# Kernel optimization log

Measured on AMD Instinct MI355X. Metric: run time of the kernel, lower is better.

The kernel has to match this reference:

```python
import jax, jax.numpy as jnp
from jax import lax
import numpy as np

B, FRAMES, H, W = 8, 128, 64, 64
N_MFCC = 60
VID_FEAT = 196
D = VID_FEAT + N_MFCC   # COMBINE_SIZE = 256
ED = 2 * D              # mamba d_inner = 512
NST = 16                # d_state
DTR = 16                # dt_rank = ceil(D/16)
NL = 4                  # layers per direction
NC = 2                  # num_classes


def setup_inputs() -> dict:
    key = jax.random.key(0)
    ks = iter(jax.random.split(key, 64))
    def rn(shape, s=0.02):
        return jax.random.normal(next(ks), shape, jnp.float32) * s
    inp = {
        'video_input': jax.random.normal(next(ks), (B, FRAMES, 3, H, W), jnp.float32),
        'audio_input': jax.random.normal(next(ks), (B, FRAMES * N_MFCC), jnp.float32),
        'cnn_conv1_w': rn((32, 3, 3, 3), 0.1), 'cnn_conv1_b': jnp.zeros((32,), jnp.float32),
        'cnn_conv2_w': rn((64, 32, 3, 3), 0.05), 'cnn_conv2_b': jnp.zeros((64,), jnp.float32),
        'cnn_fc_w': rn((VID_FEAT, 64), 0.1), 'cnn_fc_b': jnp.zeros((VID_FEAT,), jnp.float32),
    }
    for pref in ('fwd', 'bwd'):
        inp[pref + '_norm_w'] = jnp.ones((NL, D), jnp.float32)
        inp[pref + '_in_proj_w'] = rn((NL, 2 * ED, D))
        inp[pref + '_conv_w'] = rn((NL, ED, 4), 0.1)
        inp[pref + '_conv_b'] = jnp.zeros((NL, ED), jnp.float32)
        inp[pref + '_x_proj_w'] = rn((NL, DTR + 2 * NST, ED))
        inp[pref + '_dt_w'] = rn((NL, ED, DTR), 0.1)
        inp[pref + '_dt_b'] = jnp.zeros((NL, ED), jnp.float32)
        inp[pref + '_A_log'] = jnp.tile(jnp.log(jnp.arange(1, NST + 1, dtype=jnp.float32)), (NL, ED, 1))
        inp[pref + '_D'] = jnp.ones((NL, ED), jnp.float32)
        inp[pref + '_out_proj_w'] = rn((NL, D, ED))
    inp['fc_w'] = rn((D, 2 * D)); inp['fc_b'] = jnp.zeros((D,), jnp.float32)
    inp['fc2_w'] = rn((NC, D)); inp['fc2_b'] = jnp.zeros((NC,), jnp.float32)
    return inp


def _rmsnorm(x, w, eps=1e-5):
    return x * lax.rsqrt(jnp.mean(x * x, -1, keepdims=True) + eps) * w


def _conv2d(x, w, b):
    y = lax.conv_general_dilated(x, w, (1, 1), 'SAME', dimension_numbers=('NCHW', 'OIHW', 'NCHW'))
    return y + b[None, :, None, None]


def _maxpool2(x):
    return lax.reduce_window(x, -jnp.inf, lax.max, (1, 1, 2, 2), (1, 1, 2, 2), 'VALID')


def _video_cnn(x, w1, b1, w2, b2, fw, fb):
    x = _maxpool2(jax.nn.relu(_conv2d(x, w1, b1)))
    x = _maxpool2(jax.nn.relu(_conv2d(x, w2, b2)))
    x = jnp.mean(x, (2, 3))            # global avg pool -> [B*F, 64]
    return x @ fw.T + fb               # [B*F, VID_FEAT]


def _mamba_layer(x, norm_w, in_w, conv_w, conv_b, xp_w, dt_w, dt_b, A_log, Dp, out_w):
    Bsz, L, _ = x.shape
    xn = _rmsnorm(x, norm_w)
    xz = jnp.einsum('bld,ed->ble', xn, in_w)        # [B,L,2*ED]
    xc, z = jnp.split(xz, 2, axis=-1)
    # causal depthwise conv1d, kernel 4
    xpad = jnp.pad(xc, ((0, 0), (3, 0), (0, 0)))
    xc = sum(xpad[:, k:k + L, :] * conv_w[:, k] for k in range(4)) + conv_b
    xc = jax.nn.silu(xc)
    dbc = jnp.einsum('ble,re->blr', xc, xp_w)       # [B,L,DTR+2*NST]
    dt, Bm, Cm = dbc[..., :DTR], dbc[..., DTR:DTR + NST], dbc[..., DTR + NST:]
    delta = jax.nn.softplus(jnp.einsum('blr,er->ble', dt, dt_w) + dt_b)  # [B,L,ED]
    A = -jnp.exp(A_log)                             # [ED,NST]
    dA = jnp.exp(delta[..., None] * A)              # [B,L,ED,NST]
    dBx = delta[..., None] * Bm[:, :, None, :] * xc[..., None]
    def step(h, inp):
        dA_t, dBx_t, c_t = inp
        h = dA_t * h + dBx_t
        return h, jnp.einsum('ben,bn->be', h, c_t)
    h0 = jnp.zeros((Bsz, ED, NST), x.dtype)
    _, ys = lax.scan(step, h0, (dA.transpose(1, 0, 2, 3), dBx.transpose(1, 0, 2, 3), Cm.transpose(1, 0, 2)))
    y = ys.transpose(1, 0, 2) + Dp * xc
    y = y * jax.nn.silu(z)
    return x + jnp.einsum('ble,de->bld', y, out_w)


def _mamba(x, norm_w, in_w, conv_w, conv_b, xp_w, dt_w, dt_b, A_log, Dp, out_w):
    for l in range(NL):
        x = _mamba_layer(x, norm_w[l], in_w[l], conv_w[l], conv_b[l], xp_w[l],
                         dt_w[l], dt_b[l], A_log[l], Dp[l], out_w[l])
    return x


def reference(video_input, audio_input, cnn_conv1_w, cnn_conv1_b, cnn_conv2_w, cnn_conv2_b,
              cnn_fc_w, cnn_fc_b,
              fwd_norm_w, fwd_in_proj_w, fwd_conv_w, fwd_conv_b, fwd_x_proj_w, fwd_dt_w,
              fwd_dt_b, fwd_A_log, fwd_D, fwd_out_proj_w,
              bwd_norm_w, bwd_in_proj_w, bwd_conv_w, bwd_conv_b, bwd_x_proj_w, bwd_dt_w,
              bwd_dt_b, bwd_A_log, bwd_D, bwd_out_proj_w,
              fc_w, fc_b, fc2_w, fc2_b):
    bsz, frames = video_input.shape[0], video_input.shape[1]
    xv = video_input.reshape(bsz * frames, 3, H, W)
    xv = _video_cnn(xv, cnn_conv1_w, cnn_conv1_b, cnn_conv2_w, cnn_conv2_b, cnn_fc_w, cnn_fc_b)
    xv = xv.reshape(bsz, frames, VID_FEAT)
    xa = audio_input.reshape(bsz, -1, N_MFCC)       # [B, frames, N_MFCC]
    xc = jnp.concatenate([xv, xa], axis=-1)         # [B, frames, D]
    xf = _mamba(xc, fwd_norm_w, fwd_in_proj_w, fwd_conv_w, fwd_conv_b, fwd_x_proj_w,
                fwd_dt_w, fwd_dt_b, fwd_A_log, fwd_D, fwd_out_proj_w)
    xb = _mamba(xc[:, ::-1], bwd_norm_w, bwd_in_proj_w, bwd_conv_w, bwd_conv_b, bwd_x_proj_w,
                bwd_dt_w, bwd_dt_b, bwd_A_log, bwd_D, bwd_out_proj_w)[:, ::-1]
    x_last = jnp.concatenate([xf, xb], axis=-1)[:, -1, :]   # [B, 2*D]; dropout = identity (eval)
    x = x_last @ fc_w.T + fc_b
    return x @ fc2_w.T + fc2_b
```

## Files before the change

kernel.cpp:

```cpp
#include <hip/hip_runtime.h>
#include <hip/hip_bf16.h>
#include <cstdint>
#include <cstddef>

#define BATCH 8
#define FRAMES 128
#define TOK (BATCH*FRAMES)
#define NM 60
#define VF 196
#define DD 256
#define EDIM 512
#define NSTATE 16
#define DTRANK 16
#define NLAYER 4

typedef __attribute__((ext_vector_type(8))) short short8v;
typedef __attribute__((ext_vector_type(4))) float f32x4;

__device__ __forceinline__ unsigned short f2bf(float f) {
  unsigned x = __float_as_uint(f);
  unsigned r = (x + 0x7FFFu + ((x >> 16) & 1u)) >> 16;
  return (unsigned short)r;
}
__device__ __forceinline__ float bf2f(unsigned short u) {
  return __uint_as_float((unsigned)u << 16);
}

__global__ void pack_all(const float* __restrict__ ipF, const float* __restrict__ ipR,
                         const float* __restrict__ opF, const float* __restrict__ opR,
                         const float* __restrict__ xpF, const float* __restrict__ xpR,
                         const float* __restrict__ w2, const float* __restrict__ w1,
                         unsigned short* __restrict__ Wip, unsigned short* __restrict__ Wop,
                         unsigned short* __restrict__ Wxp, unsigned short* __restrict__ Wb,
                         unsigned short* __restrict__ Wb1) {
  int id = blockIdx.x * 256 + threadIdx.x;
  if (id < 262144) {
    int dl = id >> 15, r = id & 32767;
    int ntile = r >> 9, kt = (r >> 6) & 7, lane = r & 63;
    int dir = dl >> 2, layer = dl & 3;
    const float* src = (dir ? ipR : ipF) + (size_t)layer * 1024 * 256
                       + (size_t)(ntile * 16 + (lane & 15)) * 256 + kt * 32 + (lane >> 4) * 8;
    unsigned u[4];
#pragma unroll
    for (int p = 0; p < 4; ++p)
      u[p] = (unsigned)f2bf(src[2 * p]) | ((unsigned)f2bf(src[2 * p + 1]) << 16);
    uint4 v = {u[0], u[1], u[2], u[3]};
    *(uint4*)(Wip + (size_t)id * 8) = v;
  } else if (id < 262144 + 131072) {
    int id2 = id - 262144;
    int dl = id2 >> 14, rr = id2 & 16383;
    int ntile = rr >> 10, kt = (rr >> 6) & 15, lane = rr & 63;
    int dir = dl >> 2, layer = dl & 3;
    const float* src = (dir ? opR : opF) + (size_t)layer * 256 * 512
                       + (size_t)(ntile * 16 + (lane & 15)) * 512 + kt * 32 + (lane >> 4) * 8;
    unsigned u[4];
#pragma unroll
    for (int p = 0; p < 4; ++p)
      u[p] = (unsigned)f2bf(src[2 * p]) | ((unsigned)f2bf(src[2 * p + 1]) << 16);
    uint4 v = {u[0], u[1], u[2], u[3]};
    *(uint4*)(Wop + (size_t)id2 * 8) = v;
  } else if (id < 262144 + 131072 + 24576) {
    int id3 = id - 262144 - 131072;
    int dl = id3 / 3072, rr = id3 % 3072;
    int ntile = rr >> 10, kt = (rr >> 6) & 15, lane = rr & 63;
    int dir = dl >> 2, layer = dl & 3;
    const float* src = (dir ? xpR : xpF) + (size_t)layer * 48 * 512
                       + (size_t)(ntile * 16 + (lane & 15)) * 512 + kt * 32 + (lane >> 4) * 8;
    unsigned u[4];
#pragma unroll
    for (int p = 0; p < 4; ++p)
      u[p] = (unsigned)f2bf(src[2 * p]) | ((unsigned)f2bf(src[2 * p + 1]) << 16);
    uint4 v = {u[0], u[1], u[2], u[3]};
    *(uint4*)(Wxp + (size_t)id3 * 8) = v;
  } else if (id < 417792 + 2304) {
    int id4 = id - 417792;
    int lane = id4 & 63;
    int mt = (id4 >> 6) & 3;
    int sh = id4 >> 8;
    int dy = sh / 3, dx = sh % 3;
    int oc = mt * 16 + (lane & 15);
    int ic0 = (lane >> 4) * 8;
    unsigned u[4];
#pragma unroll
    for (int p = 0; p < 4; ++p) {
      unsigned short lo = f2bf(w2[((oc * 32 + ic0 + 2 * p) * 3 + dy) * 3 + dx]);
      unsigned short hi = f2bf(w2[((oc * 32 + ic0 + 2 * p + 1) * 3 + dy) * 3 + dx]);
      u[p] = (unsigned)lo | ((unsigned)hi << 16);
    }
    uint4 v = {u[0], u[1], u[2], u[3]};
    *(uint4*)(Wb + (size_t)id4 * 8) = v;
  } else if (id < 417792 + 2304 + 128) {
    int id5 = id - 417792 - 2304;
    int mt = id5 >> 6, lane = id5 & 63;
    int oc = mt * 16 + (lane & 15);
    int ko = lane >> 4;
    unsigned u[4];
#pragma unroll
    for (int p = 0; p < 4; ++p) {
      int k0 = ko * 8 + 2 * p, k1 = k0 + 1;
      unsigned short lo = (k0 < 27) ? f2bf(w1[oc * 27 + k0]) : 0;
      unsigned short hi = (k1 < 27) ? f2bf(w1[oc * 27 + k1]) : 0;
      u[p] = (unsigned)lo | ((unsigned)hi << 16);
    }
    uint4 v = {u[0], u[1], u[2], u[3]};
    *(uint4*)(Wb1 + (size_t)id5 * 8) = v;
  }
}

#define C1RS 68
#define C1ICS (66*68)
__global__ __launch_bounds__(256) void conv1_mfma(
    const float* __restrict__ video, const unsigned short* __restrict__ Wb1,
    const float* __restrict__ b1, unsigned short* __restrict__ X1)
{
  __shared__ unsigned short ldsu[3 * C1ICS + 96];
  const int img = blockIdx.x, t = threadIdx.x;
  const float* vin = video + (size_t)img * 12288;
  const int lane = t & 63, wv = t >> 6;
  const int col = lane & 15, ko = lane >> 4;

  for (int i = t; i < (3 * C1ICS + 96) / 2; i += 256) ((unsigned*)ldsu)[i] = 0;
  __syncthreads();
#pragma unroll
  for (int i = 0; i < 12; ++i) {
    int c = i * 256 + t;
    int ic = c >> 10, rem = c & 1023, gy = rem >> 4, c4 = rem & 15;
    float4 v = *(const float4*)(vin + ic * 4096 + gy * 64 + c4 * 4);
    unsigned lo = (unsigned)f2bf(v.x) | ((unsigned)f2bf(v.y) << 16);
    unsigned hi = (unsigned)f2bf(v.z) | ((unsigned)f2bf(v.w) << 16);
    int di = ic * C1ICS + (gy + 1) * C1RS + 4 + c4 * 4;
    *(uint2*)(ldsu + di) = (uint2){lo, hi};
  }

  short8v A0 = *(const short8v*)(Wb1 + (size_t)(0 * 64 + lane) * 8);
  short8v A1 = *(const short8v*)(Wb1 + (size_t)(1 * 64 + lane) * 8);
  float bia[2][4];
#pragma unroll
  for (int mt = 0; mt < 2; ++mt)
#pragma unroll
    for (int r = 0; r < 4; ++r) bia[mt][r] = b1[mt * 16 + ko * 4 + r];

  int offs[8];
#pragma unroll
  for (int j = 0; j < 8; ++j) {
    int k = ko * 8 + j;
    int o = 0;
    if (k < 27) {
      int ic = k / 9, tap = k - ic * 9;
      int dy = tap / 3, dx = tap - dy * 3;
      o = ic * C1ICS + dy * C1RS + dx + 3;
    }
    offs[j] = o;
  }
  __syncthreads();

  f32x4 z4 = {0.f, 0.f, 0.f, 0.f};
#pragma unroll 1
  for (int rp = 0; rp < 8; ++rp) {
    const int y0 = wv * 16 + rp * 2;
#pragma unroll
    for (int xg = 0; xg < 4; ++xg) {
      const int bse = y0 * C1RS + xg * 16 + col;
      short8v vb0, vb1;
#pragma unroll
      for (int j = 0; j < 8; ++j) {
        vb0[j] = (short)ldsu[bse + offs[j]];
        vb1[j] = (short)ldsu[bse + C1RS + offs[j]];
      }
      f32x4 c00 = __builtin_amdgcn_mfma_f32_16x16x32_bf16(A0, vb0, z4, 0, 0, 0);
      f32x4 c10 = __builtin_amdgcn_mfma_f32_16x16x32_bf16(A1, vb0, z4, 0, 0, 0);
      f32x4 c01 = __builtin_amdgcn_mfma_f32_16x16x32_bf16(A0, vb1, z4, 0, 0, 0);
      f32x4 c11 = __builtin_amdgcn_mfma_f32_16x16x32_bf16(A1, vb1, z4, 0, 0, 0);
      const int py = wv * 8 + rp;
      const int pxp = xg * 8 + (col >> 1);
#pragma unroll
      for (int mt = 0; mt < 2; ++mt) {
        f32x4 ca = mt ? c10 : c00;
        f32x4 cb = mt ? c11 : c01;
        unsigned pk[2];
#pragma unroll
        for (int r = 0; r < 4; ++r) {
          float va = fmaxf(ca[r] + bia[mt][r], 0.f);
          float vb = fmaxf(cb[r] + bia[mt][r], 0.f);
          float v = fmaxf(va, vb);
          v = fmaxf(v, __shfl_xor(v, 1, 64));
          unsigned short u = f2bf(v);
          if ((r & 1) == 0) pk[r >> 1] = (unsigned)u;
          else              pk[r >> 1] |= ((unsigned)u << 16);
        }
        if ((col & 1) == 0) {
          uint2 o = {pk[0], pk[1]};
          *(uint2*)(X1 + ((size_t)(img * 1024 + py * 32 + pxp) * 32 + mt * 16 + ko * 4)) = o;
        }
      }
    }
  }
}

#define OCT_STRIDE  (1156 * 16 + 32)
#define X_LDS_BYTES (4 * OCT_STRIDE)
__global__ __launch_bounds__(256) void conv2_k(
    const unsigned short* __restrict__ X1, const unsigned short* __restrict__ Wb,
    const float* __restrict__ b2, float* __restrict__ feat)
{
  extern __shared__ char sm[];
  float* part = (float*)(sm + X_LDS_BYTES);
  const int img = blockIdx.x, t = threadIdx.x;
  const int lane = t & 63, wv = t >> 6;
  const int kg = lane >> 4, l15 = lane & 15;

  for (int j = t; j < 1156; j += 256) {
    int r = j / 34, cc = j - r * 34;
    if (r == 0 || r == 33 || cc == 0 || cc == 33) {
      uint4 z = {0, 0, 0, 0};
#pragma unroll
      for (int oct = 0; oct < 4; ++oct)
        *(uint4*)(sm + oct * OCT_STRIDE + j * 16) = z;
    }
  }
  const uint4* src = (const uint4*)(X1 + (size_t)img * 32768);
#pragma unroll 4
  for (int i = 0; i < 16; ++i) {
    int c = i * 256 + t;
    uint4 v = src[c];
    int oct = c & 3, P = c >> 2;
    int y = P >> 5, x = P & 31;
    *(uint4*)(sm + oct * OCT_STRIDE + ((y + 1) * 34 + (x + 1)) * 16) = v;
  }
  __syncthreads();

  float bia[4][4];
#pragma unroll
  for (int mt = 0; mt < 4; ++mt)
#pragma unroll
    for (int r = 0; r < 4; ++r) bia[mt][r] = b2[mt * 16 + kg * 4 + r];

  float msum[4][4];
#pragma unroll
  for (int mt = 0; mt < 4; ++mt)
#pragma unroll
    for (int r = 0; r < 4; ++r) msum[mt][r] = 0.f;

#pragma unroll 1
  for (int pass = 0; pass < 2; ++pass) {
#pragma unroll 1
    for (int hf = 0; hf < 2; ++hf) {
#pragma unroll 1
      for (int qq = 0; qq < 2; ++qq) {
        f32x4 acc[4][2];
#pragma unroll
        for (int mt = 0; mt < 4; ++mt) {
          acc[mt][0] = (f32x4){0.f, 0.f, 0.f, 0.f};
          acc[mt][1] = (f32x4){0.f, 0.f, 0.f, 0.f};
        }
        int Pq[2];
#pragma unroll
        for (int j = 0; j < 2; ++j) {
          int qsel = qq + j * 2;
          int p = (wv * 16 + pass * 8 + hf * 4 + qsel) * 16 + l15;
          int y = p >> 5, x = p & 31;
          Pq[j] = y * 34 + x;
        }
#pragma unroll
        for (int sh = 0; sh < 9; ++sh) {
          const int dy = sh / 3, dx = sh % 3;
          const int shoff = (dy * 34 + dx) * 16;
          short8v Af[4];
#pragma unroll
          for (int mt = 0; mt < 4; ++mt)
            Af[mt] = *(const short8v*)(Wb + ((size_t)(sh * 4 + mt) * 64 + lane) * 8);
          short8v B0 = *(const short8v*)(sm + kg * OCT_STRIDE + Pq[0] * 16 + shoff);
          short8v B1 = *(const short8v*)(sm + kg * OCT_STRIDE + Pq[1] * 16 + shoff);
#pragma unroll
          for (int mt = 0; mt < 4; ++mt) {
            acc[mt][0] = __builtin_amdgcn_mfma_f32_16x16x32_bf16(Af[mt], B0, acc[mt][0], 0, 0, 0);
            acc[mt][1] = __builtin_amdgcn_mfma_f32_16x16x32_bf16(Af[mt], B1, acc[mt][1], 0, 0, 0);
          }
        }
#pragma unroll
        for (int mt = 0; mt < 4; ++mt)
#pragma unroll
          for (int r = 0; r < 4; ++r) {
            float va = fmaxf(acc[mt][0][r] + bia[mt][r], 0.f);
            float vb = fmaxf(acc[mt][1][r] + bia[mt][r], 0.f);
            float v = fmaxf(va, vb);
            v = fmaxf(v, __shfl_xor(v, 1, 64));
            msum[mt][r] += v;
          }
      }
    }
  }
#pragma unroll
  for (int mt = 0; mt < 4; ++mt)
#pragma unroll
    for (int r = 0; r < 4; ++r) {
      float v = msum[mt][r];
      v += __shfl_xor(v, 1, 64);
      v += __shfl_xor(v, 2, 64);
      v += __shfl_xor(v, 4, 64);
      v += __shfl_xor(v, 8, 64);
      if (l15 == 0) part[wv * 64 + mt * 16 + kg * 4 + r] = v * 0.5f;
    }
  __syncthreads();
  if (t < 64)
    feat[(size_t)img * 64 + t] =
        (part[t] + part[64 + t] + part[128 + t] + part[192 + t]) * (1.f / 256.f);
}

__global__ __launch_bounds__(256) void fcgemm_k(
    const float* __restrict__ A, const float* __restrict__ B,
    const float* __restrict__ bias, const float* __restrict__ audio,
    float* __restrict__ xf, float* __restrict__ xr)
{
  __shared__ float sA[16][68];
  __shared__ float sB[16][68];
  const int t = threadIdx.x;
  const int m0 = blockIdx.x * 64;
  const int n0 = blockIdx.y * 64;
  const int tx = t & 15, ty = t >> 4;
  const int lk = t & 15, lr = t >> 4;
  float acc[4][4] = {};
  for (int k0 = 0; k0 < 64; k0 += 16) {
#pragma unroll
    for (int rr = 0; rr < 4; ++rr) {
      int m = m0 + lr + rr * 16;
      sA[lk][lr + rr * 16] = A[(size_t)m * 64 + k0 + lk];
      int n = n0 + lr + rr * 16;
      sB[lk][lr + rr * 16] = (n < VF) ? B[(size_t)n * 64 + k0 + lk] : 0.f;
    }
    __syncthreads();
#pragma unroll
    for (int kk = 0; kk < 16; ++kk) {
      float a0 = sA[kk][ty*4+0], a1 = sA[kk][ty*4+1], a2 = sA[kk][ty*4+2], a3 = sA[kk][ty*4+3];
      float b0 = sB[kk][tx*4+0], b1 = sB[kk][tx*4+1], b2 = sB[kk][tx*4+2], b3 = sB[kk][tx*4+3];
      acc[0][0]=fmaf(a0,b0,acc[0][0]); acc[0][1]=fmaf(a0,b1,acc[0][1]); acc[0][2]=fmaf(a0,b2,acc[0][2]); acc[0][3]=fmaf(a0,b3,acc[0][3]);
      acc[1][0]=fmaf(a1,b0,acc[1][0]); acc[1][1]=fmaf(a1,b1,acc[1][1]); acc[1][2]=fmaf(a1,b2,acc[1][2]); acc[1][3]=fmaf(a1,b3,acc[1][3]);
      acc[2][0]=fmaf(a2,b0,acc[2][0]); acc[2][1]=fmaf(a2,b1,acc[2][1]); acc[2][2]=fmaf(a2,b2,acc[2][2]); acc[2][3]=fmaf(a2,b3,acc[2][3]);
      acc[3][0]=fmaf(a3,b0,acc[3][0]); acc[3][1]=fmaf(a3,b1,acc[3][1]); acc[3][2]=fmaf(a3,b2,acc[3][2]); acc[3][3]=fmaf(a3,b3,acc[3][3]);
    }
    __syncthreads();
  }
#pragma unroll
  for (int i = 0; i < 4; ++i) {
    int m = m0 + ty * 4 + i;
    int b = m >> 7, l = m & 127;
    int mr = (b << 7) + (127 - l);
#pragma unroll
    for (int j = 0; j < 4; ++j) {
      int n = n0 + tx * 4 + j;
      float v;
      if (n < VF)       v = acc[i][j] + bias[n];
      else              v = audio[(size_t)b * (FRAMES * NM) + l * NM + (n - VF)];
      xf[(size_t)m * DD + n] = v;
      xr[(size_t)mr * DD + n] = v;
    }
  }
}

__global__ __launch_bounds__(256) void inproj_mfma3(
    const float* __restrict__ xF, const float* __restrict__ xR,
    const float* __restrict__ nwF, const float* __restrict__ nwR,
    const unsigned short* __restrict__ Wip, int layer,
    unsigned short* __restrict__ xzF, unsigned short* __restrict__ xzR)
{
  const int dir = blockIdx.z;
  const float* x = dir ? xR : xF;
  const float* nw = dir ? nwR : nwF;
  unsigned short* xz = dir ? xzR : xzF;
  __shared__ unsigned short sa[32 * 16 * 8];
  const int t = threadIdx.x;
  const int tok0 = blockIdx.x * 16;
  {
    const int tk = t >> 4, l16 = t & 15;
    const float* row = x + (size_t)(tok0 + tk) * DD + l16 * 16;
    float v[16];
    float ss = 0.f;
#pragma unroll
    for (int i = 0; i < 4; ++i) {
      float4 f = ((const float4*)row)[i];
      v[4*i] = f.x; v[4*i+1] = f.y; v[4*i+2] = f.z; v[4*i+3] = f.w;
      ss += f.x*f.x + f.y*f.y + f.z*f.z + f.w*f.w;
    }
    ss += __shfl_xor(ss, 1, 16);
    ss += __shfl_xor(ss, 2, 16);
    ss += __shfl_xor(ss, 4, 16);
    ss += __shfl_xor(ss, 8, 16);
    float scale = rsqrtf(ss * (1.f / DD) + 1e-5f);
    const float* nwp = nw + l16 * 16;
#pragma unroll
    for (int hh = 0; hh < 2; ++hh) {
      unsigned ub[4];
#pragma unroll
      for (int p = 0; p < 4; ++p) {
        unsigned short lo = f2bf(v[hh*8 + 2*p]     * scale * nwp[hh*8 + 2*p]);
        unsigned short hi = f2bf(v[hh*8 + 2*p + 1] * scale * nwp[hh*8 + 2*p + 1]);
        ub[p] = (unsigned)lo | ((unsigned)hi << 16);
      }
      int k0 = l16 * 16 + hh * 8;
      int kt = k0 >> 5, oct = (k0 >> 3) & 3;
      uint4 w4 = {ub[0], ub[1], ub[2], ub[3]};
      *(uint4*)(sa + ((size_t)(kt * 4 + oct) * 16 + tk) * 8) = w4;
    }
  }
  __syncthreads();
  const int lane = t & 63, w = t >> 6;
  short8v af[8];
#pragma unroll
  for (int kt = 0; kt < 8; ++kt)
    af[kt] = *(const short8v*)(sa + ((size_t)(kt * 4 + (lane >> 4)) * 16 + (lane & 15)) * 8);
#pragma unroll
  for (int ns = 0; ns < 4; ++ns) {
    const int ntile = blockIdx.y * 16 + w * 4 + ns;
    const unsigned short* wb = Wip + (((size_t)(dir * 4 + layer) * 512 + ntile * 8) * 64 + lane) * 8;
    f32x4 acc = (f32x4){0.f, 0.f, 0.f, 0.f};
#pragma unroll
    for (int kt = 0; kt < 8; ++kt) {
      short8v bf = *(const short8v*)(wb + (size_t)kt * 64 * 8);
      acc = __builtin_amdgcn_mfma_f32_16x16x32_bf16(af[kt], bf, acc, 0, 0, 0);
    }
#pragma unroll
    for (int r = 0; r < 4; ++r)
      xz[(size_t)(tok0 + (lane >> 4) * 4 + r) * 1024 + ntile * 16 + (lane & 15)] = f2bf(acc[r]);
  }
}

__global__ __launch_bounds__(256) void xprojf_k(
    const unsigned short* __restrict__ xzF, const unsigned short* __restrict__ xzR,
    const float* __restrict__ cwF, const float* __restrict__ cwR,
    const float* __restrict__ cbF, const float* __restrict__ cbR,
    const unsigned short* __restrict__ Wxp, int layer,
    float* __restrict__ xcF, float* __restrict__ xcR,
    float* __restrict__ dbF, float* __restrict__ dbR)
{
  const int dir = blockIdx.z;
  const unsigned short* xz = dir ? xzR : xzF;
  const float* cw = dir ? cwR : cwF;
  const float* cb = dir ? cbR : cbF;
  float* xc = dir ? xcR : xcF;
  float* db = dir ? dbR : dbF;
  __shared__ unsigned short sa[64 * 16 * 8];
  const int t = threadIdx.x;
  const int tok0 = blockIdx.x * 16;

#pragma unroll
  for (int ii = 0; ii < 4; ++ii) {
    int idx = ii * 256 + t;
    int tk = idx >> 6, tok = tok0 + tk;
    int e0 = (idx & 63) << 3;
    int l = tok & 127;
    const unsigned short* col = xz + (size_t)tok * 1024 + e0;

    unsigned short v3[8] = {}, v2[8] = {}, v1[8] = {}, v0[8];
    if (l >= 3) *(uint4*)v3 = *(const uint4*)(col - 3 * 1024);
    if (l >= 2) *(uint4*)v2 = *(const uint4*)(col - 2 * 1024);
    if (l >= 1) *(uint4*)v1 = *(const uint4*)(col - 1 * 1024);
    *(uint4*)v0 = *(const uint4*)col;

    float cbv[8];
    *(float4*)cbv = *(const float4*)(cb + e0); *(float4*)(cbv+4) = *(const float4*)(cb + e0 + 4);

    float res[8];
#pragma unroll
    for (int j = 0; j < 8; ++j) {
      float4 cv = ((const float4*)cw)[e0 + j];
      float a = cbv[j];
      a = fmaf(cv.x, bf2f(v3[j]), a);
      a = fmaf(cv.y, bf2f(v2[j]), a);
      a = fmaf(cv.z, bf2f(v1[j]), a);
      a = fmaf(cv.w, bf2f(v0[j]), a);
      res[j] = a / (1.f + __expf(-a));
    }
    float4 r0 = {res[0], res[1], res[2], res[3]};
    float4 r1 = {res[4], res[5], res[6], res[7]};
    float* xcp = xc + (size_t)tok * EDIM + e0;
    *(float4*)xcp = r0; *(float4*)(xcp + 4) = r1;

    unsigned ub[4];
#pragma unroll
    for (int p = 0; p < 4; ++p)
      ub[p] = (unsigned)f2bf(res[2*p]) | ((unsigned)f2bf(res[2*p+1]) << 16);
    int c = (e0 >> 3) * 16 + tk;
    c ^= (c >> 4) & 15;
    uint4 w4 = {ub[0], ub[1], ub[2], ub[3]};
    *(uint4*)(sa + (size_t)c * 8) = w4;
  }
  __syncthreads();

  const int w = t >> 6, lane = t & 63;
  if (w < 3) {
    const int nt = w;
    const unsigned short* wbase = Wxp + ((size_t)(dir * 4 + layer) * 3 * 16 * 64) * 8;
    f32x4 acc = (f32x4){0.f, 0.f, 0.f, 0.f};
#pragma unroll
    for (int kt = 0; kt < 16; ++kt) {
      int c = (kt * 4 + (lane >> 4)) * 16 + (lane & 15);
      c ^= (c >> 4) & 15;
      short8v af = *(const short8v*)(sa + (size_t)c * 8);
      short8v bf = *(const short8v*)(wbase + ((size_t)(nt * 16 + kt) * 64 + lane) * 8);
      acc = __builtin_amdgcn_mfma_f32_16x16x32_bf16(af, bf, acc, 0, 0, 0);
    }
#pragma unroll
    for (int r = 0; r < 4; ++r)
      db[(size_t)(tok0 + (lane >> 4) * 4 + r) * 48 + nt * 16 + (lane & 15)] = acc[r];
  }
}

__global__ __launch_bounds__(256) void scan4_k(
    const unsigned short* __restrict__ xzF, const unsigned short* __restrict__ xzR,
    const float* __restrict__ xcF, const float* __restrict__ xcR,
    const float* __restrict__ dbF, const float* __restrict__ dbR,
    const float* __restrict__ dwF, const float* __restrict__ dwR,
    const float* __restrict__ dtbF, const float* __restrict__ dtbR,
    const float* __restrict__ AlF, const float* __restrict__ AlR,
    const float* __restrict__ DpF, const float* __restrict__ DpR,
    unsigned short* __restrict__ yoF, unsigned short* __restrict__ yoR)
{
  const int dir = blockIdx.z;
  const unsigned short* xz = dir ? xzR : xzF;
  const float* xc = dir ? xcR : xcF;
  const float* db = dir ? dbR : dbF;
  const float* dw = dir ? dwR : dwF;
  const float* dtbv = dir ? dtbR : dtbF;
  const float* Al = dir ? AlR : AlF;
  const float* Dp = dir ? DpR : DpF;
  unsigned short* yo = dir ? yoR : yoF;

  __shared__ float sdb[FRAMES * 48];
  __shared__ float sxc[FRAMES * 16];
  __shared__ float sgz[FRAMES * 16];
  __shared__ float sdl[FRAMES * 16];
  const int b = blockIdx.x >> 5;
  const int e0 = (blockIdx.x & 31) << 4;
  const int t = threadIdx.x, g = t >> 4, n = t & 15;
  const int e = e0 + g;

  const float* dbp = db + (size_t)b * FRAMES * 48;
  for (int i = t; i < FRAMES * 48 / 4; i += 256)
    ((float4*)sdb)[i] = ((const float4*)dbp)[i];
  for (int i = t; i < FRAMES * 16; i += 256) {
    int l = i >> 4, c = i & 15;
    int ee = e0 + c;
    sxc[i] = xc[(size_t)(b * FRAMES + l) * EDIM + ee];
    float zz = bf2f(xz[(size_t)(b * FRAMES + l) * 1024 + 512 + ee]);
    sgz[i] = zz / (1.f + __expf(-zz));
    const float* d = db + (size_t)(b * FRAMES + l) * 48;
    const float* w = dw + (size_t)ee * 16;
    float a = dtbv[ee];
#pragma unroll
    for (int q = 0; q < 4; ++q) {
      float4 dv = *(const float4*)(d + 4 * q);
      float4 wv = *(const float4*)(w + 4 * q);
      a = fmaf(dv.x, wv.x, a); a = fmaf(dv.y, wv.y, a);
      a = fmaf(dv.z, wv.z, a); a = fmaf(dv.w, wv.w, a);
    }
    sdl[i] = (a > 20.f) ? a : __logf(1.f + __expf(a));
  }
  float An = -expf(Al[e * NSTATE + n]);
  float Dv = Dp[e];
  float h = 0.f;
  unsigned short* yp = yo + ((size_t)((e >> 5) * 4 + ((e >> 3) & 3)) * 1024 + b * FRAMES) * 8 + (e & 7);
  __syncthreads();

#pragma unroll 1
  for (int l = 0; l < FRAMES; ++l) {
    float dlt = sdl[l * 16 + g];
    float xcv = sxc[l * 16 + g];
    float Bn = sdb[l * 48 + 16 + n];
    float Cn = sdb[l * 48 + 32 + n];
    float dA = __expf(dlt * An);
    h = fmaf(dA, h, dlt * xcv * Bn);
    float part = h * Cn;
    part += __shfl_xor(part, 1, 16);
    part += __shfl_xor(part, 2, 16);
    part += __shfl_xor(part, 4, 16);
    part += __shfl_xor(part, 8, 16);
    if (n == 0) {
      float a2 = fmaf(Dv, xcv, part);
      yp[(size_t)l * 8] = f2bf(a2 * sgz[l * 16 + g]);
    }
  }
}

__global__ __launch_bounds__(256) void outproj_mfma(
    const unsigned short* __restrict__ yoF, const unsigned short* __restrict__ yoR,
    const unsigned short* __restrict__ Wop, int layer,
    float* __restrict__ xF, float* __restrict__ xR)
{
  const int dir = blockIdx.z;
  const unsigned short* yo = dir ? yoR : yoF;
  float* xx = dir ? xR : xF;
  const int t = threadIdx.x, lane = t & 63, w = t >> 6;
  const int m0 = blockIdx.x * 32, n0 = blockIdx.y * 64;
  const int ntile = blockIdx.y * 4 + w;
  const unsigned short* wb = Wop + (((size_t)(dir * 4 + layer) * 256 + ntile * 16) * 64 + lane) * 8;
  f32x4 acc[2];
  acc[0] = (f32x4){0.f, 0.f, 0.f, 0.f};
  acc[1] = (f32x4){0.f, 0.f, 0.f, 0.f};
#pragma unroll
  for (int kt = 0; kt < 16; ++kt) {
    short8v bf = *(const short8v*)(wb + (size_t)kt * 64 * 8);
#pragma unroll
    for (int mt = 0; mt < 2; ++mt) {
      short8v af = *(const short8v*)(yo + ((size_t)(kt * 4 + (lane >> 4)) * 1024 + m0 + mt * 16 + (lane & 15)) * 8);
      acc[mt] = __builtin_amdgcn_mfma_f32_16x16x32_bf16(af, bf, acc[mt], 0, 0, 0);
    }
  }
#pragma unroll
  for (int mt = 0; mt < 2; ++mt)
#pragma unroll
    for (int r = 0; r < 4; ++r) {
      size_t ci = (size_t)(m0 + mt * 16 + (lane >> 4) * 4 + r) * DD + n0 + w * 16 + (lane & 15);
      xx[ci] += acc[mt][r];
    }
}

__global__ __launch_bounds__(256) void head_k(
    const float* __restrict__ xf, const float* __restrict__ xr,
    const float* __restrict__ fcw, const float* __restrict__ fcb,
    const float* __restrict__ fc2w, const float* __restrict__ fc2b,
    float* __restrict__ out)
{
  int b = blockIdx.x;
  __shared__ float xl[2 * DD];
  __shared__ float h[DD];
  __shared__ float hp[4];
  int t = threadIdx.x;
  xl[t]      = xf[(size_t)(b * FRAMES + FRAMES - 1) * DD + t];
  xl[DD + t] = xr[(size_t)(b * FRAMES + 0) * DD + t];
  __syncthreads();
  float acc = fcb[t];
  for (int k = 0; k < 2 * DD; ++k) acc = fmaf(xl[k], fcw[(size_t)t * 2 * DD + k], acc);
  h[t] = acc;
  __syncthreads();
  {
    int c = t >> 7, k = t & 127;
    float p = h[k] * fc2w[c * DD + k] + h[k + 128] * fc2w[c * DD + k + 128];
#pragma unroll
    for (int off = 32; off; off >>= 1) p += __shfl_xor(p, off, 64);
    if ((t & 63) == 0) hp[t >> 6] = p;
  }
  __syncthreads();
  if (t < 2) out[b * 2 + t] = hp[2 * t] + hp[2 * t + 1] + fc2b[t];
}

extern "C" void kernel_launch(void* const* d_in, const int* in_sizes, int n_in,
                              void* d_out, int out_size, void* d_ws, size_t ws_size,
                              hipStream_t stream) {
  const float* video = (const float*)d_in[0];
  const float* audio = (const float*)d_in[1];
  const float* c1w = (const float*)d_in[2];
  const float* c1b = (const float*)d_in[3];
  const float* c2w = (const float*)d_in[4];
  const float* c2b = (const float*)d_in[5];
  const float* fcw = (const float*)d_in[6];
  const float* fcb = (const float*)d_in[7];
  const float* Wf[10]; const float* Wb_[10];
  for (int i = 0; i < 10; ++i) { Wf[i] = (const float*)d_in[8+i]; Wb_[i] = (const float*)d_in[18+i]; }
  const float* fc_w  = (const float*)d_in[28];
  const float* fc_b  = (const float*)d_in[29];
  const float* fc2_w = (const float*)d_in[30];
  const float* fc2_b = (const float*)d_in[31];
  float* out = (float*)d_out;

  float* ws   = (float*)d_ws;
  float* feat = ws;
  float* xf   = feat + 65536;
  float* xr   = xf   + 262144;
  unsigned short* xzF = (unsigned short*)(xr + 262144);
  unsigned short* xzR = (unsigned short*)(xr + 262144 + 1048576);
  float* xcF  = xr + 262144 + 2097152;
  float* xcR  = xcF  + 524288;
  float* dbF  = xcR  + 524288;
  float* dbR  = dbF  + 49152;
  unsigned short* yoF = (unsigned short*)(dbR + 49152);
  unsigned short* yoR = yoF + 524288;
  unsigned short* X1  = yoR + 524288;
  unsigned short* Wbp = X1 + 33554432;
  unsigned short* Wip = Wbp + 18432;
  unsigned short* Wop = Wip + 2097152;
  unsigned short* Wxp = Wop + 1048576;
  unsigned short* Wb1 = Wxp + 196608;

  pack_all<<<dim3(1642), 256, 0, stream>>>(Wf[1], Wb_[1], Wf[9], Wb_[9], Wf[4], Wb_[4],
                                           c2w, c1w, Wip, Wop, Wxp, Wbp, Wb1);
  conv1_mfma<<<dim3(TOK), 256, 0, stream>>>(video, Wb1, c1b, X1);
  conv2_k<<<dim3(TOK), 256, (size_t)(X_LDS_BYTES + 1024), stream>>>(X1, Wbp, c2b, feat);

  fcgemm_k<<<dim3(16, 4), 256, 0, stream>>>(feat, fcw, fcb, audio, xf, xr);

  for (int l = 0; l < NLAYER; ++l) {
    const float* nwF  = Wf[0] + l*DD;              const float* nwR  = Wb_[0] + l*DD;
    const float* cwF_ = Wf[2] + l*EDIM*4;          const float* cwR_ = Wb_[2] + l*EDIM*4;
    const float* cbF_ = Wf[3] + l*EDIM;            const float* cbR_ = Wb_[3] + l*EDIM;
    const float* dwF  = Wf[5] + l*EDIM*DTRANK;     const float* dwR  = Wb_[5] + l*EDIM*DTRANK;
    const float* dtbF = Wf[6] + l*EDIM;            const float* dtbR = Wb_[6] + l*EDIM;
    const float* AlF  = Wf[7] + l*EDIM*NSTATE;     const float* AlR  = Wb_[7] + l*EDIM*NSTATE;
    const float* DpF  = Wf[8] + l*EDIM;            const float* DpR  = Wb_[8] + l*EDIM;

    inproj_mfma3<<<dim3(64, 4, 2), 256, 0, stream>>>(xf, xr, nwF, nwR, Wip, l, xzF, xzR);
    xprojf_k<<<dim3(64, 1, 2), 256, 0, stream>>>(xzF, xzR, cwF_, cwR_, cbF_, cbR_,
                                                 Wxp, l, xcF, xcR, dbF, dbR);
    scan4_k<<<dim3(256, 1, 2), 256, 0, stream>>>(xzF, xzR, xcF, xcR, dbF, dbR, dwF, dwR,
                                                 dtbF, dtbR, AlF, AlR, DpF, DpR, yoF, yoR);
    outproj_mfma<<<dim3(32, 4, 2), 256, 0, stream>>>(yoF, yoR, Wop, l, xf, xr);
  }

  head_k<<<dim3(BATCH), 256, 0, stream>>>(xf, xr, fc_w, fc_b, fc2_w, fc2_b, out);
}
```

Baseline: 349.4 us.

## Split conv2 per image across two blocks with XOR-swizzled LDS and atomic accumulation

conv2_k now runs two blocks per image, each covering half the rows (17 padded rows instead of 34). The LDS tile uses a compact 32-byte-per-pixel layout with an XOR swizzle to avoid bank conflicts, replacing the per-octet planes with padding. The goal is to roughly halve LDS per block, raising occupancy and grid parallelism. Partial means are combined with atomicAdd into feat, which now needs a memset first. conv1 LDS padding also changes to a fixed 4496 stride.

```diff
diff --git a/kernel.cpp b/kernel.cpp
--- a/kernel.cpp
+++ b/kernel.cpp
@@ -108,7 +108,7 @@
 }
 
 #define C1RS 68
-#define C1ICS (66*68)
+#define C1ICS 4496
 __global__ __launch_bounds__(256) void conv1_mfma(
     const float* __restrict__ video, const unsigned short* __restrict__ Wb1,
     const float* __restrict__ b1, unsigned short* __restrict__ X1)
@@ -197,35 +197,43 @@
   }
 }
 
-#define OCT_STRIDE  (1156 * 16 + 32)
-#define X_LDS_BYTES (4 * OCT_STRIDE)
+#define C2LDS (18 * 34 * 32)
 __global__ __launch_bounds__(256) void conv2_k(
     const unsigned short* __restrict__ X1, const unsigned short* __restrict__ Wb,
     const float* __restrict__ b2, float* __restrict__ feat)
 {
-  extern __shared__ char sm[];
-  float* part = (float*)(sm + X_LDS_BYTES);
-  const int img = blockIdx.x, t = threadIdx.x;
+  __shared__ unsigned short xs[C2LDS];
+  __shared__ float part[256];
+  const int img = blockIdx.x >> 1, h = blockIdx.x & 1;
+  const int t = threadIdx.x;
   const int lane = t & 63, wv = t >> 6;
   const int kg = lane >> 4, l15 = lane & 15;
 
-  for (int j = t; j < 1156; j += 256) {
-    int r = j / 34, cc = j - r * 34;
-    if (r == 0 || r == 33 || cc == 0 || cc == 33) {
-      uint4 z = {0, 0, 0, 0};
-#pragma unroll
-      for (int oct = 0; oct < 4; ++oct)
-        *(uint4*)(sm + oct * OCT_STRIDE + j * 16) = z;
-    }
-  }
-  const uint4* src = (const uint4*)(X1 + (size_t)img * 32768);
-#pragma unroll 4
-  for (int i = 0; i < 16; ++i) {
-    int c = i * 256 + t;
-    uint4 v = src[c];
-    int oct = c & 3, P = c >> 2;
-    int y = P >> 5, x = P & 31;
-    *(uint4*)(sm + oct * OCT_STRIDE + ((y + 1) * 34 + (x + 1)) * 16) = v;
+  {
+    uint4 z = {0, 0, 0, 0};
+    uint4* dst = (uint4*)xs;
+    const int rz = h ? 17 : 0;
+    for (int j = t; j < 70; j += 256) {
+      int r, c;
+      if (j < 36) { r = j >> 1; c = (j & 1) ? 33 : 0; }
+      else        { r = rz;     c = j - 36; }
+      int px = r * 34 + c;
+#pragma unroll
+      for (int g = 0; g < 4; ++g)
+        dst[(px * 4 + g) ^ (px & 7)] = z;
+    }
+  }
+  {
+    const uint4* src = (const uint4*)(X1 + (size_t)img * 32768);
+    uint4* dst = (uint4*)xs;
+    for (int i = t; i < 17 * 128; i += 256) {
+      int vr = i >> 7, rem = i & 127;
+      int c = rem >> 2, g = rem & 3;
+      int x1row = h ? (15 + vr) : vr;
+      int ldsRow = h ? vr : (vr + 1);
+      int px = ldsRow * 34 + c + 1;
+      dst[(px * 4 + g) ^ (px & 7)] = src[(x1row * 32 + c) * 4 + g];
+    }
   }
   __syncthreads();
 
@@ -242,52 +250,53 @@
     for (int r = 0; r < 4; ++r) msum[mt][r] = 0.f;
 
 #pragma unroll 1
-  for (int pass = 0; pass < 2; ++pass) {
+  for (int hf = 0; hf < 2; ++hf) {
 #pragma unroll 1
-    for (int hf = 0; hf < 2; ++hf) {
-#pragma unroll 1
-      for (int qq = 0; qq < 2; ++qq) {
-        f32x4 acc[4][2];
+    for (int qq = 0; qq < 2; ++qq) {
+      f32x4 acc[4][2];
+#pragma unroll
+      for (int mt = 0; mt < 4; ++mt) {
+        acc[mt][0] = (f32x4){0.f, 0.f, 0.f, 0.f};
+        acc[mt][1] = (f32x4){0.f, 0.f, 0.f, 0.f};
+      }
+      int Pq[2];
+#pragma unroll
+      for (int j = 0; j < 2; ++j) {
+        int qsel = qq + j * 2;
+        int p = (wv * 8 + hf * 4 + qsel) * 16 + l15;
+        int ly = p >> 5, x = p & 31;
+        Pq[j] = ly * 34 + x;
+      }
+#pragma unroll
+      for (int sh = 0; sh < 9; ++sh) {
+        const int dy = sh / 3, dx = sh % 3;
+        const int off = dy * 34 + dx;
+        short8v Af[4];
+#pragma unroll
+        for (int mt = 0; mt < 4; ++mt)
+          Af[mt] = *(const short8v*)(Wb + ((size_t)(sh * 4 + mt) * 64 + lane) * 8);
+        int p0 = Pq[0] + off;
+        int c0 = (p0 * 4 + kg) ^ (p0 & 7);
+        short8v B0 = *(const short8v*)(xs + (size_t)c0 * 8);
+        int p1 = Pq[1] + off;
+        int c1 = (p1 * 4 + kg) ^ (p1 & 7);
+        short8v B1 = *(const short8v*)(xs + (size_t)c1 * 8);
 #pragma unroll
         for (int mt = 0; mt < 4; ++mt) {
-          acc[mt][0] = (f32x4){0.f, 0.f, 0.f, 0.f};
-          acc[mt][1] = (f32x4){0.f, 0.f, 0.f, 0.f};
+          acc[mt][0] = __builtin_amdgcn_mfma_f32_16x16x32_bf16(Af[mt], B0, acc[mt][0], 0, 0, 0);
+          acc[mt][1] = __builtin_amdgcn_mfma_f32_16x16x32_bf16(Af[mt], B1, acc[mt][1], 0, 0, 0);
         }
-        int Pq[2];
-#pragma unroll
-        for (int j = 0; j < 2; ++j) {
-          int qsel = qq + j * 2;
-          int p = (wv * 16 + pass * 8 + hf * 4 + qsel) * 16 + l15;
-          int y = p >> 5, x = p & 31;
-          Pq[j] = y * 34 + x;
+      }
+#pragma unroll
+      for (int mt = 0; mt < 4; ++mt)
+#pragma unroll
+        for (int r = 0; r < 4; ++r) {
+          float va = fmaxf(acc[mt][0][r] + bia[mt][r], 0.f);
+          float vb = fmaxf(acc[mt][1][r] + bia[mt][r], 0.f);
+          float v = fmaxf(va, vb);
+          v = fmaxf(v, __shfl_xor(v, 1, 64));
+          msum[mt][r] += v;
         }
-#pragma unroll
-        for (int sh = 0; sh < 9; ++sh) {
-          const int dy = sh / 3, dx = sh % 3;
-          const int shoff = (dy * 34 + dx) * 16;
-          short8v Af[4];
-#pragma unroll
-          for (int mt = 0; mt < 4; ++mt)
-            Af[mt] = *(const short8v*)(Wb + ((size_t)(sh * 4 + mt) * 64 + lane) * 8);
-          short8v B0 = *(const short8v*)(sm + kg * OCT_STRIDE + Pq[0] * 16 + shoff);
-          short8v B1 = *(const short8v*)(sm + kg * OCT_STRIDE + Pq[1] * 16 + shoff);
-#pragma unroll
-          for (int mt = 0; mt < 4; ++mt) {
-            acc[mt][0] = __builtin_amdgcn_mfma_f32_16x16x32_bf16(Af[mt], B0, acc[mt][0], 0, 0, 0);
-            acc[mt][1] = __builtin_amdgcn_mfma_f32_16x16x32_bf16(Af[mt], B1, acc[mt][1], 0, 0, 0);
-          }
-        }
-#pragma unroll
-        for (int mt = 0; mt < 4; ++mt)
-#pragma unroll
-          for (int r = 0; r < 4; ++r) {
-            float va = fmaxf(acc[mt][0][r] + bia[mt][r], 0.f);
-            float vb = fmaxf(acc[mt][1][r] + bia[mt][r], 0.f);
-            float v = fmaxf(va, vb);
-            v = fmaxf(v, __shfl_xor(v, 1, 64));
-            msum[mt][r] += v;
-          }
-      }
     }
   }
 #pragma unroll
@@ -303,8 +312,8 @@
     }
   __syncthreads();
   if (t < 64)
-    feat[(size_t)img * 64 + t] =
-        (part[t] + part[64 + t] + part[128 + t] + part[192 + t]) * (1.f / 256.f);
+    atomicAdd(&feat[(size_t)img * 64 + t],
+              (part[t] + part[64 + t] + part[128 + t] + part[192 + t]) * (1.f / 256.f));
 }
 
 __global__ __launch_bounds__(256) void fcgemm_k(
@@ -681,10 +690,11 @@
   unsigned short* Wxp = Wop + 1048576;
   unsigned short* Wb1 = Wxp + 196608;
 
+  hipMemsetAsync(feat, 0, (size_t)TOK * 64 * sizeof(float), stream);
   pack_all<<<dim3(1642), 256, 0, stream>>>(Wf[1], Wb_[1], Wf[9], Wb_[9], Wf[4], Wb_[4],
                                            c2w, c1w, Wip, Wop, Wxp, Wbp, Wb1);
   conv1_mfma<<<dim3(TOK), 256, 0, stream>>>(video, Wb1, c1b, X1);
-  conv2_k<<<dim3(TOK), 256, (size_t)(X_LDS_BYTES + 1024), stream>>>(X1, Wbp, c2b, feat);
+  conv2_k<<<dim3(TOK * 2), 256, 0, stream>>>(X1, Wbp, c2b, feat);
 
   fcgemm_k<<<dim3(16, 4), 256, 0, stream>>>(feat, fcw, fcb, audio, xf, xr);
 
```

Result: slower. 399.3 us (+14.3%).
